# Kernel tuning notes

Hardware: AMD Instinct MI355X
Metric: run time of the kernel (lower is better)

The kernel has to match this reference:

```python
import jax, jax.numpy as jnp
import numpy as np

D_MODEL = 1024
N_HEADS = 16
D_HEAD = 64
INIT_RANGE = 0.02
IGNORE = -100000.0


def setup_inputs() -> dict:
    key = jax.random.key(0)
    ks = jax.random.split(key, 5)
    x = jax.random.normal(ks[0], (2, 2048, D_MODEL), dtype=jnp.float32)
    W_Q = jax.random.normal(ks[1], (N_HEADS, D_MODEL, D_HEAD), dtype=jnp.float32) * INIT_RANGE
    W_K = jax.random.normal(ks[2], (N_HEADS, D_MODEL, D_HEAD), dtype=jnp.float32) * INIT_RANGE
    W_V = jax.random.normal(ks[3], (N_HEADS, D_MODEL, D_HEAD), dtype=jnp.float32) * INIT_RANGE
    W_O = jax.random.normal(ks[4], (N_HEADS, D_HEAD, D_MODEL), dtype=jnp.float32) * INIT_RANGE
    b_Q = jnp.zeros((N_HEADS, D_HEAD), dtype=jnp.float32)
    b_K = jnp.zeros((N_HEADS, D_HEAD), dtype=jnp.float32)
    b_V = jnp.zeros((N_HEADS, D_HEAD), dtype=jnp.float32)
    b_O = jnp.zeros((D_MODEL,), dtype=jnp.float32)
    return {"normalized_resid_pre": x, "W_Q": W_Q, "W_K": W_K, "W_V": W_V,
            "W_O": W_O, "b_Q": b_Q, "b_K": b_K, "b_V": b_V, "b_O": b_O}


def reference(normalized_resid_pre, W_Q, W_K, W_V, W_O, b_Q, b_K, b_V, b_O):
    x = normalized_resid_pre  # [b, s, d_model]
    q = jnp.einsum('bsd,hde->bshe', x, W_Q) + b_Q  # [b, s, h, d_head]
    k = jnp.einsum('bsd,hde->bshe', x, W_K) + b_K
    v = jnp.einsum('bsd,hde->bshe', x, W_V) + b_V
    scores = jnp.einsum('bqhe,bkhe->bhqk', q, k) / jnp.sqrt(jnp.float32(D_HEAD))
    s = x.shape[1]
    causal = jnp.arange(s)[:, None] >= jnp.arange(s)[None, :]  # [q, k]
    scores = jnp.where(causal, scores, jnp.float32(IGNORE))
    pattern = jax.nn.softmax(scores, axis=-1)  # [b, h, q, k]
    z = jnp.einsum('bkhe,bhqk->bqhe', v, pattern)
    out = jnp.einsum('bqhe,hed->bqd', z, W_O) + b_O
    return out
```

## Files before the change

### kernel.cpp

```cpp
#include <hip/hip_runtime.h>

#define SEQ 2048
#define BATCH 2
#define DM 1024
#define NH 16
#define DH 64

typedef __bf16 bf16;
typedef __bf16 bf16x8 __attribute__((ext_vector_type(8)));
typedef __bf16 bf16x4 __attribute__((ext_vector_type(4)));
typedef float f32x4 __attribute__((ext_vector_type(4)));

#define MFMA16(a, b, c) __builtin_amdgcn_mfma_f32_16x16x32_bf16((a), (b), (c), 0, 0, 0)

#if __has_builtin(__builtin_amdgcn_exp2f)
#define EXP2(x) __builtin_amdgcn_exp2f(x)
#else
#define EXP2(x) exp2f(x)
#endif

#define QSCALE 0.18033688f

typedef __attribute__((address_space(3))) void lds_void;
typedef __attribute__((address_space(1))) void glb_void;
__device__ __forceinline__ void gld16(void* lds, const void* g) {
    __builtin_amdgcn_global_load_lds((const glb_void*)g, (lds_void*)lds, 16, 0, 0);
}

__global__ __launch_bounds__(256) void k_prep(const float* __restrict__ x,
                                              const float* __restrict__ WQ,
                                              const float* __restrict__ WK,
                                              const float* __restrict__ WV,
                                              const float* __restrict__ WO,
                                              bf16* __restrict__ xb,
                                              bf16* __restrict__ wT,
                                              bf16* __restrict__ woT) {
    int bx = blockIdx.x;
    int t = threadIdx.x;
    if (bx < 2048) {
        int g = bx * 256 + t;
        const float4* x4 = (const float4*)x;
        float4 a = x4[2 * g];
        float4 b = x4[2 * g + 1];
        bf16x8 o;
        o[0] = (bf16)a.x; o[1] = (bf16)a.y; o[2] = (bf16)a.z; o[3] = (bf16)a.w;
        o[4] = (bf16)b.x; o[5] = (bf16)b.y; o[6] = (bf16)b.z; o[7] = (bf16)b.w;
        *(bf16x8*)(xb + 8 * g) = o;
        return;
    }
    __shared__ bf16 T[64 * 65];
    if (bx < 2816) {
        int id = bx - 2048;
        int kt = id & 15, ph = id >> 4;
        int p = ph >> 4, h = ph & 15;
        const float* Wp = (p == 0) ? WQ : (p == 1) ? WK : WV;
        const float* src = Wp + ((size_t)h * DM + (size_t)kt * 64) * DH;
        for (int i = 0; i < 4; i++) {
            int c = t + 256 * i;
            int r = c >> 4;
            int col = (c & 15) * 4;
            float4 v = *(const float4*)&src[r * 64 + col];
            T[(col + 0) * 65 + r] = (bf16)v.x;
            T[(col + 1) * 65 + r] = (bf16)v.y;
            T[(col + 2) * 65 + r] = (bf16)v.z;
            T[(col + 3) * 65 + r] = (bf16)v.w;
        }
        __syncthreads();
        bf16* dst = wT + (size_t)ph * 64 * DM + (size_t)kt * 64;
        for (int i = 0; i < 2; i++) {
            int c = t + 256 * i;
            int e = c >> 3;
            int k0 = (c & 7) * 8;
            bf16x8 o;
            for (int j = 0; j < 8; j++) o[j] = T[e * 65 + k0 + j];
            *(bf16x8*)&dst[(size_t)e * DM + k0] = o;
        }
    } else {
        int id = bx - 2816;
        int ht = id & 15, dt = id >> 4;
        for (int i = 0; i < 4; i++) {
            int c = t + 256 * i;
            int r = c >> 4;
            int col = (c & 15) * 4;
            float4 v = *(const float4*)&WO[((size_t)(ht * 64 + r)) * DM + dt * 64 + col];
            T[(col + 0) * 65 + r] = (bf16)v.x;
            T[(col + 1) * 65 + r] = (bf16)v.y;
            T[(col + 2) * 65 + r] = (bf16)v.z;
            T[(col + 3) * 65 + r] = (bf16)v.w;
        }
        __syncthreads();
        for (int i = 0; i < 2; i++) {
            int c = t + 256 * i;
            int d = c >> 3;
            int h0 = (c & 7) * 8;
            bf16x8 o;
            for (int j = 0; j < 8; j++) o[j] = T[d * 65 + h0 + j];
            *(bf16x8*)&woT[((size_t)(dt * 64 + d)) * DM + ht * 64 + h0] = o;
        }
    }
}

__global__ __launch_bounds__(256, 4) void k_qkv(const bf16* __restrict__ xb,
                                                const bf16* __restrict__ wT,
                                                const float* __restrict__ bQ,
                                                const float* __restrict__ bK,
                                                const float* __restrict__ bV,
                                                bf16* __restrict__ Qb,
                                                bf16* __restrict__ Kb,
                                                bf16* __restrict__ VTf) {
    int mt = blockIdx.x, nt = blockIdx.y, p = blockIdx.z;
    __shared__ __align__(16) bf16 Xs[16 * 512];
    __shared__ __align__(16) bf16 Ws[16 * 512];
    int t = threadIdx.x;
    int lane = t & 63, w = t >> 6;
    int l15 = lane & 15, quad = lane >> 4;

    const f32x4 z4 = {0.f, 0.f, 0.f, 0.f};
    f32x4 acc[2][8];
    for (int mi = 0; mi < 2; mi++)
        for (int ni = 0; ni < 8; ni++) acc[mi][ni] = z4;

    int m0 = mt * 128, n0 = nt * 128;
    const bf16* xrow = xb + (size_t)m0 * DM;
    const bf16* wrow = wT + ((size_t)p * 1024 + n0) * DM;

    for (int k0 = 0; k0 < DM; k0 += 64) {
        __syncthreads();
        for (int i = 0; i < 4; i++) {
            int f = w + 4 * i;
            int ks = f >> 3, ni = f & 7;
            size_t off = (size_t)(ni * 16 + l15) * DM + k0 + ks * 32 + quad * 8;
            gld16(Xs + f * 512, xrow + off);
            gld16(Ws + f * 512, wrow + off);
        }
        __syncthreads();
        for (int ks = 0; ks < 2; ks++) {
            bf16x8 a0 = *(const bf16x8*)&Xs[(ks * 8 + w * 2 + 0) * 512 + lane * 8];
            bf16x8 a1 = *(const bf16x8*)&Xs[(ks * 8 + w * 2 + 1) * 512 + lane * 8];
            for (int ni = 0; ni < 8; ni++) {
                bf16x8 bfr = *(const bf16x8*)&Ws[(ks * 8 + ni) * 512 + lane * 8];
                acc[0][ni] = MFMA16(a0, bfr, acc[0][ni]);
                acc[1][ni] = MFMA16(a1, bfr, acc[1][ni]);
            }
        }
    }

    int b = mt >> 4;
    int kt = mt & 15;
    int s00 = kt * 128;
    if (p < 2) {
        const float* bias = (p == 0) ? bQ : bK;
        bf16* dst = (p == 0) ? Qb : Kb;
        float scale = (p == 0) ? QSCALE : 1.0f;
        for (int ni = 0; ni < 8; ni++) {
            int he = n0 + ni * 16 + l15;
            int h = he >> 6, e = he & 63;
            float bia = bias[he];
            size_t rb = (size_t)(b * NH + h) * SEQ * DH + e;
            for (int mi = 0; mi < 2; mi++)
                for (int r = 0; r < 4; r++) {
                    int s = s00 + w * 32 + mi * 16 + quad * 4 + r;
                    dst[rb + (size_t)s * DH] = (bf16)((acc[mi][ni][r] + bia) * scale);
                }
        }
    } else {
        for (int ni = 0; ni < 8; ni++) {
            int he = n0 + ni * 16 + l15;
            int h = he >> 6, e = he & 63;
            int no = (e >> 4) & 3;
            float bia = bV[he];
            size_t base = (((size_t)(b * NH + h) * 16 + kt) * 16 + (w * 4 + no)) * 512
                          + (size_t)((quad << 4) | l15) * 8;
            for (int mi = 0; mi < 2; mi++) {
                bf16x4 o;
                for (int r = 0; r < 4; r++) o[r] = (bf16)(acc[mi][ni][r] + bia);
                *(bf16x4*)&VTf[base + mi * 4] = o;
            }
        }
    }
}

__global__ __launch_bounds__(512, 4) void k_attn(const bf16* __restrict__ Qb,
                                                 const bf16* __restrict__ Kb,
                                                 const bf16* __restrict__ VTf,
                                                 bf16* __restrict__ Zb) {
    int bh = blockIdx.x;
    int y = blockIdx.y;
    int qt = (y < 8) ? y : 23 - y;
    int h = bh & 15, b = bh >> 4;
    __shared__ __align__(16) bf16 Ks[2][16 * 512];
    __shared__ __align__(16) bf16 Vs[16 * 512];
    int t = threadIdx.x;
    int lane = t & 63, w = t >> 6;
    int l15 = lane & 15, quad = lane >> 4;

    const bf16* qbase = Qb + (size_t)bh * SEQ * DH;
    const bf16* kbase = Kb + (size_t)bh * SEQ * DH;
    const bf16* vfrag = VTf + (size_t)bh * 16 * 8192;

    int qr0 = qt * 128 + w * 16;
    bf16x8 aq[2];
    for (int ks = 0; ks < 2; ks++)
        aq[ks] = *(const bf16x8*)&qbase[(size_t)(qr0 + l15) * DH + ks * 32 + quad * 8];

    auto stageK = [&](int buf, int kt) {
        for (int i = 0; i < 2; i++) {
            int f = w * 2 + i;
            int ks = f >> 3, ni = f & 7;
            gld16(&Ks[buf][f * 512],
                  kbase + (size_t)(kt * 128 + ni * 16 + l15) * DH + ks * 32 + quad * 8);
        }
    };
    auto stageV = [&](int kt) {
        const bf16* vt = vfrag + (size_t)kt * 8192;
        for (int i = 0; i < 2; i++) {
            int f = w * 2 + i;
            gld16(&Vs[f * 512], vt + f * 512 + lane * 8);
        }
    };

    const bf16 one = (bf16)1.0f;
    const bf16x8 ones = {one, one, one, one, one, one, one, one};
    const f32x4 z4 = {0.f, 0.f, 0.f, 0.f};
    f32x4 acco[4], accd;
    for (int no = 0; no < 4; no++) acco[no] = z4;
    accd = z4;

    stageK(0, 0);

    for (int kt = 0; kt <= qt; kt++) {
        int buf = kt & 1;
        __syncthreads();
        stageV(kt);
        if (kt < qt) stageK(buf ^ 1, kt + 1);
        const bf16* Kbuf = Ks[buf];

        f32x4 accs[8];
        for (int ni = 0; ni < 8; ni++) accs[ni] = z4;
        for (int ks = 0; ks < 2; ks++)
            for (int ni = 0; ni < 8; ni++) {
                bf16x8 ak = *(const bf16x8*)&Kbuf[(ks * 8 + ni) * 512 + lane * 8];
                accs[ni] = MFMA16(ak, aq[ks], accs[ni]);
            }

        if (kt == qt) {
            int ql = w * 16 + l15;
            for (int ni = 0; ni < 8; ni++) {
                int kvl = ni * 16 + quad * 4;
                for (int r = 0; r < 4; r++)
                    if (kvl + r > ql) accs[ni][r] = -1e30f;
            }
        }

        bf16x4 pt[8];
        for (int ni = 0; ni < 8; ni++)
            for (int r = 0; r < 4; r++)
                pt[ni][r] = (bf16)EXP2(accs[ni][r]);

        __syncthreads();

        for (int p4 = 0; p4 < 4; p4++) {
            bf16x8 ap;
            for (int j = 0; j < 4; j++) {
                ap[j] = pt[2 * p4][j];
                ap[4 + j] = pt[2 * p4 + 1][j];
            }
            accd = MFMA16(ap, ones, accd);
            for (int no = 0; no < 4; no++) {
                bf16x8 bv = *(const bf16x8*)&Vs[(p4 * 4 + no) * 512 + lane * 8];
                acco[no] = MFMA16(ap, bv, acco[no]);
            }
        }
    }

    for (int r = 0; r < 4; r++) {
        float inv = 1.0f / accd[r];
        int q = qr0 + quad * 4 + r;
        size_t rowbase = ((size_t)b * SEQ + q) * DM + h * DH;
        for (int no = 0; no < 4; no++)
            Zb[rowbase + no * 16 + l15] = (bf16)(acco[no][r] * inv);
    }
}

__global__ __launch_bounds__(256, 4) void k_out(const bf16* __restrict__ Zb,
                                                const bf16* __restrict__ woT,
                                                const float* __restrict__ bO,
                                                float* __restrict__ out) {
    int mt = blockIdx.x;
    int nt = blockIdx.y;
    __shared__ __align__(16) bf16 Xs[16 * 512];
    __shared__ __align__(16) bf16 Ws[8 * 512];
    int t = threadIdx.x;
    int lane = t & 63, w = t >> 6;
    int l15 = lane & 15, quad = lane >> 4;

    int m0 = mt * 128, n0 = nt * 64;
    const bf16* zrow = Zb + (size_t)m0 * DM;
    const bf16* wrow = woT + (size_t)n0 * DM;

    const f32x4 z4 = {0.f, 0.f, 0.f, 0.f};
    f32x4 acc[2][4];
    for (int mi = 0; mi < 2; mi++)
        for (int ni = 0; ni < 4; ni++) acc[mi][ni] = z4;

    for (int k0 = 0; k0 < DM; k0 += 64) {
        __syncthreads();
        for (int i = 0; i < 4; i++) {
            int f = w + 4 * i;
            int ks = f >> 3, ni = f & 7;
            gld16(Xs + f * 512,
                  zrow + (size_t)(ni * 16 + l15) * DM + k0 + ks * 32 + quad * 8);
        }
        for (int i = 0; i < 2; i++) {
            int f = w * 2 + i;
            int ks = f >> 2, ni = f & 3;
            gld16(Ws + f * 512,
                  wrow + (size_t)(ni * 16 + l15) * DM + k0 + ks * 32 + quad * 8);
        }
        __syncthreads();
        for (int ks = 0; ks < 2; ks++) {
            bf16x8 a0 = *(const bf16x8*)&Xs[(ks * 8 + w * 2 + 0) * 512 + lane * 8];
            bf16x8 a1 = *(const bf16x8*)&Xs[(ks * 8 + w * 2 + 1) * 512 + lane * 8];
            for (int ni = 0; ni < 4; ni++) {
                bf16x8 bfr = *(const bf16x8*)&Ws[(ks * 4 + ni) * 512 + lane * 8];
                acc[0][ni] = MFMA16(a0, bfr, acc[0][ni]);
                acc[1][ni] = MFMA16(a1, bfr, acc[1][ni]);
            }
        }
    }
    for (int ni = 0; ni < 4; ni++) {
        int d = n0 + ni * 16 + l15;
        float bia = bO[d];
        for (int mi = 0; mi < 2; mi++)
            for (int r = 0; r < 4; r++) {
                int s = m0 + w * 32 + mi * 16 + quad * 4 + r;
                out[(size_t)s * DM + d] = acc[mi][ni][r] + bia;
            }
    }
}

extern "C" void kernel_launch(void* const* d_in, const int* in_sizes, int n_in,
                              void* d_out, int out_size, void* d_ws, size_t ws_size,
                              hipStream_t stream) {
    const float* x  = (const float*)d_in[0];
    const float* WQ = (const float*)d_in[1];
    const float* WK = (const float*)d_in[2];
    const float* WV = (const float*)d_in[3];
    const float* WO = (const float*)d_in[4];
    const float* bQ = (const float*)d_in[5];
    const float* bK = (const float*)d_in[6];
    const float* bV = (const float*)d_in[7];
    const float* bO = (const float*)d_in[8];
    float* out = (float*)d_out;

    char* w = (char*)d_ws;
    bf16* xb    = (bf16*)(w + 0);
    bf16* wqkvT = (bf16*)(w + (8u << 20));
    bf16* woT   = (bf16*)(w + (14u << 20));
    bf16* Qb    = (bf16*)(w + (16u << 20));
    bf16* Kb    = (bf16*)(w + (24u << 20));
    bf16* VTf   = (bf16*)(w + (32u << 20));
    bf16* Zb    = (bf16*)(w + (40u << 20));

    k_prep<<<3072, 256, 0, stream>>>(x, WQ, WK, WV, WO, xb, wqkvT, woT);
    k_qkv<<<dim3(32, 8, 3), 256, 0, stream>>>(xb, wqkvT, bQ, bK, bV, Qb, Kb, VTf);
    k_attn<<<dim3(32, 16), 512, 0, stream>>>(Qb, Kb, VTf, Zb);
    k_out<<<dim3(32, 16), 256, 0, stream>>>(Zb, woT, bO, out);
}
```

Before: 199.4 us.

## Shrink QKV and output GEMM tiles, swap operands for vectorized stores

The QKV projection tile drops from 128x128 to 128x64 (one head per block), and the output projection tile drops from 128x64 to 64x64. This doubles the grid sizes and allows higher occupancy through launch bounds of 6. For Q/K, and for the output GEMM, the MFMA operands are swapped so each lane holds four consecutive output columns, which lets the epilogues use bf16x4 and float4 vector stores instead of scalar strided stores. The trade-off is less operand reuse per loaded tile, which means more global and LDS traffic per FLOP.

```diff
diff --git a/kernel.cpp b/kernel.cpp
--- a/kernel.cpp
+++ b/kernel.cpp
@@ -100,7 +100,7 @@
     }
 }
 
-__global__ __launch_bounds__(256, 4) void k_qkv(const bf16* __restrict__ xb,
+__global__ __launch_bounds__(256, 6) void k_qkv(const bf16* __restrict__ xb,
                                                 const bf16* __restrict__ wT,
                                                 const float* __restrict__ bQ,
                                                 const float* __restrict__ bK,
@@ -110,70 +110,89 @@
                                                 bf16* __restrict__ VTf) {
     int mt = blockIdx.x, nt = blockIdx.y, p = blockIdx.z;
     __shared__ __align__(16) bf16 Xs[16 * 512];
-    __shared__ __align__(16) bf16 Ws[16 * 512];
+    __shared__ __align__(16) bf16 Ws[8 * 512];
     int t = threadIdx.x;
     int lane = t & 63, w = t >> 6;
     int l15 = lane & 15, quad = lane >> 4;
 
     const f32x4 z4 = {0.f, 0.f, 0.f, 0.f};
-    f32x4 acc[2][8];
-    for (int mi = 0; mi < 2; mi++)
-        for (int ni = 0; ni < 8; ni++) acc[mi][ni] = z4;
-
-    int m0 = mt * 128, n0 = nt * 128;
+    f32x4 acc[8];
+    for (int i = 0; i < 8; i++) acc[i] = z4;
+
+    int m0 = mt * 128;
     const bf16* xrow = xb + (size_t)m0 * DM;
-    const bf16* wrow = wT + ((size_t)p * 1024 + n0) * DM;
+    const bf16* wrow = wT + ((size_t)p * 1024 + nt * 64) * DM;
 
     for (int k0 = 0; k0 < DM; k0 += 64) {
         __syncthreads();
-        for (int i = 0; i < 4; i++) {
+        for (int i = 0; i < 6; i++) {
             int f = w + 4 * i;
-            int ks = f >> 3, ni = f & 7;
-            size_t off = (size_t)(ni * 16 + l15) * DM + k0 + ks * 32 + quad * 8;
-            gld16(Xs + f * 512, xrow + off);
-            gld16(Ws + f * 512, wrow + off);
-        }
-        __syncthreads();
-        for (int ks = 0; ks < 2; ks++) {
-            bf16x8 a0 = *(const bf16x8*)&Xs[(ks * 8 + w * 2 + 0) * 512 + lane * 8];
-            bf16x8 a1 = *(const bf16x8*)&Xs[(ks * 8 + w * 2 + 1) * 512 + lane * 8];
-            for (int ni = 0; ni < 8; ni++) {
-                bf16x8 bfr = *(const bf16x8*)&Ws[(ks * 8 + ni) * 512 + lane * 8];
-                acc[0][ni] = MFMA16(a0, bfr, acc[0][ni]);
-                acc[1][ni] = MFMA16(a1, bfr, acc[1][ni]);
+            if (f < 16) {
+                int ks = f >> 3, ni = f & 7;
+                gld16(Xs + f * 512,
+                      xrow + (size_t)(ni * 16 + l15) * DM + k0 + ks * 32 + quad * 8);
+            } else {
+                int g = f - 16;
+                int ks = g >> 2, ni = g & 3;
+                gld16(Ws + g * 512,
+                      wrow + (size_t)(ni * 16 + l15) * DM + k0 + ks * 32 + quad * 8);
+            }
+        }
+        __syncthreads();
+        if (p < 2) {
+            for (int ks = 0; ks < 2; ks++) {
+                bf16x8 b0 = *(const bf16x8*)&Xs[(ks * 8 + w * 2 + 0) * 512 + lane * 8];
+                bf16x8 b1 = *(const bf16x8*)&Xs[(ks * 8 + w * 2 + 1) * 512 + lane * 8];
+                for (int mi = 0; mi < 4; mi++) {
+                    bf16x8 a = *(const bf16x8*)&Ws[(ks * 4 + mi) * 512 + lane * 8];
+                    acc[mi * 2 + 0] = MFMA16(a, b0, acc[mi * 2 + 0]);
+                    acc[mi * 2 + 1] = MFMA16(a, b1, acc[mi * 2 + 1]);
+                }
+            }
+        } else {
+            for (int ks = 0; ks < 2; ks++) {
+                bf16x8 a0 = *(const bf16x8*)&Xs[(ks * 8 + w * 2 + 0) * 512 + lane * 8];
+                bf16x8 a1 = *(const bf16x8*)&Xs[(ks * 8 + w * 2 + 1) * 512 + lane * 8];
+                for (int ni = 0; ni < 4; ni++) {
+                    bf16x8 b = *(const bf16x8*)&Ws[(ks * 4 + ni) * 512 + lane * 8];
+                    acc[0 * 4 + ni] = MFMA16(a0, b, acc[0 * 4 + ni]);
+                    acc[1 * 4 + ni] = MFMA16(a1, b, acc[1 * 4 + ni]);
+                }
             }
         }
     }
 
     int b = mt >> 4;
     int kt = mt & 15;
-    int s00 = kt * 128;
     if (p < 2) {
         const float* bias = (p == 0) ? bQ : bK;
         bf16* dst = (p == 0) ? Qb : Kb;
         float scale = (p == 0) ? QSCALE : 1.0f;
-        for (int ni = 0; ni < 8; ni++) {
-            int he = n0 + ni * 16 + l15;
-            int h = he >> 6, e = he & 63;
-            float bia = bias[he];
-            size_t rb = (size_t)(b * NH + h) * SEQ * DH + e;
-            for (int mi = 0; mi < 2; mi++)
-                for (int r = 0; r < 4; r++) {
-                    int s = s00 + w * 32 + mi * 16 + quad * 4 + r;
-                    dst[rb + (size_t)s * DH] = (bf16)((acc[mi][ni][r] + bia) * scale);
-                }
+        bf16* hb = dst + (size_t)(b * NH + nt) * SEQ * DH;
+        for (int mi = 0; mi < 4; mi++) {
+            int e0 = mi * 16 + quad * 4;
+            float4 b4 = *(const float4*)&bias[nt * 64 + e0];
+            for (int nf = 0; nf < 2; nf++) {
+                int s = kt * 128 + w * 32 + nf * 16 + l15;
+                f32x4 a = acc[mi * 2 + nf];
+                bf16x4 o;
+                o[0] = (bf16)((a[0] + b4.x) * scale);
+                o[1] = (bf16)((a[1] + b4.y) * scale);
+                o[2] = (bf16)((a[2] + b4.z) * scale);
+                o[3] = (bf16)((a[3] + b4.w) * scale);
+                *(bf16x4*)&hb[(size_t)s * DH + e0] = o;
+            }
         }
     } else {
-        for (int ni = 0; ni < 8; ni++) {
-            int he = n0 + ni * 16 + l15;
-            int h = he >> 6, e = he & 63;
-            int no = (e >> 4) & 3;
-            float bia = bV[he];
-            size_t base = (((size_t)(b * NH + h) * 16 + kt) * 16 + (w * 4 + no)) * 512
+        for (int ni = 0; ni < 4; ni++) {
+            int e = ni * 16 + l15;
+            float bia = bV[nt * 64 + e];
+            size_t base = (((size_t)(b * NH + nt) * 16 + kt) * 16 + (w * 4 + ni)) * 512
                           + (size_t)((quad << 4) | l15) * 8;
             for (int mi = 0; mi < 2; mi++) {
+                f32x4 a = acc[mi * 4 + ni];
                 bf16x4 o;
-                for (int r = 0; r < 4; r++) o[r] = (bf16)(acc[mi][ni][r] + bia);
+                for (int r = 0; r < 4; r++) o[r] = (bf16)(a[r] + bia);
                 *(bf16x4*)&VTf[base + mi * 4] = o;
             }
         }
@@ -282,60 +301,60 @@
     }
 }
 
-__global__ __launch_bounds__(256, 4) void k_out(const bf16* __restrict__ Zb,
+__global__ __launch_bounds__(256, 6) void k_out(const bf16* __restrict__ Zb,
                                                 const bf16* __restrict__ woT,
                                                 const float* __restrict__ bO,
                                                 float* __restrict__ out) {
     int mt = blockIdx.x;
     int nt = blockIdx.y;
-    __shared__ __align__(16) bf16 Xs[16 * 512];
+    __shared__ __align__(16) bf16 Zs[8 * 512];
     __shared__ __align__(16) bf16 Ws[8 * 512];
     int t = threadIdx.x;
     int lane = t & 63, w = t >> 6;
     int l15 = lane & 15, quad = lane >> 4;
 
-    int m0 = mt * 128, n0 = nt * 64;
+    int m0 = mt * 64, n0 = nt * 64;
     const bf16* zrow = Zb + (size_t)m0 * DM;
     const bf16* wrow = woT + (size_t)n0 * DM;
 
     const f32x4 z4 = {0.f, 0.f, 0.f, 0.f};
-    f32x4 acc[2][4];
-    for (int mi = 0; mi < 2; mi++)
-        for (int ni = 0; ni < 4; ni++) acc[mi][ni] = z4;
+    f32x4 acc[4];
+    for (int mi = 0; mi < 4; mi++) acc[mi] = z4;
 
     for (int k0 = 0; k0 < DM; k0 += 64) {
         __syncthreads();
         for (int i = 0; i < 4; i++) {
             int f = w + 4 * i;
-            int ks = f >> 3, ni = f & 7;
-            gld16(Xs + f * 512,
-                  zrow + (size_t)(ni * 16 + l15) * DM + k0 + ks * 32 + quad * 8);
-        }
-        for (int i = 0; i < 2; i++) {
-            int f = w * 2 + i;
-            int ks = f >> 2, ni = f & 3;
-            gld16(Ws + f * 512,
-                  wrow + (size_t)(ni * 16 + l15) * DM + k0 + ks * 32 + quad * 8);
+            if (f < 8) {
+                int ks = f >> 2, ni = f & 3;
+                gld16(Zs + f * 512,
+                      zrow + (size_t)(ni * 16 + l15) * DM + k0 + ks * 32 + quad * 8);
+            } else {
+                int g = f - 8;
+                int ks = g >> 2, ni = g & 3;
+                gld16(Ws + g * 512,
+                      wrow + (size_t)(ni * 16 + l15) * DM + k0 + ks * 32 + quad * 8);
+            }
         }
         __syncthreads();
         for (int ks = 0; ks < 2; ks++) {
-            bf16x8 a0 = *(const bf16x8*)&Xs[(ks * 8 + w * 2 + 0) * 512 + lane * 8];
-            bf16x8 a1 = *(const bf16x8*)&Xs[(ks * 8 + w * 2 + 1) * 512 + lane * 8];
-            for (int ni = 0; ni < 4; ni++) {
-                bf16x8 bfr = *(const bf16x8*)&Ws[(ks * 4 + ni) * 512 + lane * 8];
-                acc[0][ni] = MFMA16(a0, bfr, acc[0][ni]);
-                acc[1][ni] = MFMA16(a1, bfr, acc[1][ni]);
-            }
-        }
-    }
-    for (int ni = 0; ni < 4; ni++) {
-        int d = n0 + ni * 16 + l15;
-        float bia = bO[d];
-        for (int mi = 0; mi < 2; mi++)
-            for (int r = 0; r < 4; r++) {
-                int s = m0 + w * 32 + mi * 16 + quad * 4 + r;
-                out[(size_t)s * DM + d] = acc[mi][ni][r] + bia;
-            }
+            bf16x8 bz = *(const bf16x8*)&Zs[(ks * 4 + w) * 512 + lane * 8];
+            for (int mi = 0; mi < 4; mi++) {
+                bf16x8 a = *(const bf16x8*)&Ws[(ks * 4 + mi) * 512 + lane * 8];
+                acc[mi] = MFMA16(a, bz, acc[mi]);
+            }
+        }
+    }
+    int s = m0 + w * 16 + l15;
+    for (int mi = 0; mi < 4; mi++) {
+        int d = n0 + mi * 16 + quad * 4;
+        float4 b4 = *(const float4*)&bO[d];
+        float4 o;
+        o.x = acc[mi][0] + b4.x;
+        o.y = acc[mi][1] + b4.y;
+        o.z = acc[mi][2] + b4.z;
+        o.w = acc[mi][3] + b4.w;
+        *(float4*)&out[(size_t)s * DM + d] = o;
     }
 }
 
@@ -363,7 +382,7 @@
     bf16* Zb    = (bf16*)(w + (40u << 20));
 
     k_prep<<<3072, 256, 0, stream>>>(x, WQ, WK, WV, WO, xb, wqkvT, woT);
-    k_qkv<<<dim3(32, 8, 3), 256, 0, stream>>>(xb, wqkvT, bQ, bK, bV, Qb, Kb, VTf);
+    k_qkv<<<dim3(32, 16, 3), 256, 0, stream>>>(xb, wqkvT, bQ, bK, bV, Qb, Kb, VTf);
     k_attn<<<dim3(32, 16), 512, 0, stream>>>(Qb, Kb, VTf, Zb);
-    k_out<<<dim3(32, 16), 256, 0, stream>>>(Zb, woT, bO, out);
-}
+    k_out<<<dim3(64, 16), 256, 0, stream>>>(Zb, woT, bO, out);
+}
```

After: 377.6 us. 89.3% more time.
